# Kernel tuning notes

Hardware: AMD Instinct MI355X
Metric: run time of the kernel (lower is better)

## Reference

```python
import jax, jax.numpy as jnp
import numpy as np

B, NORB, N_UP, N_DN, HIDDEN = 1024, 128, 32, 32, 4096


def setup_inputs() -> dict:
    rng = np.random.default_rng(0)
    # Build valid occupancy configs: exactly N_UP up-electrons (bit 0) and
    # N_DN down-electrons (bit 1) per sample. Encoding: 0=empty,1=up,2=dn,3=updn.
    up_order = np.argsort(rng.random((B, NORB)), axis=1)
    dn_order = np.argsort(rng.random((B, NORB)), axis=1)
    up_bit = np.zeros((B, NORB), np.int32)
    dn_bit = np.zeros((B, NORB), np.int32)
    np.put_along_axis(up_bit, up_order[:, :N_UP], 1, axis=1)
    np.put_along_axis(dn_bit, dn_order[:, :N_DN], 1, axis=1)
    x = jnp.asarray(up_bit + 2 * dn_bit, dtype=jnp.int32)

    key = jax.random.key(0)
    k1, k2, k3 = jax.random.split(key, 3)
    orbitals = jax.random.normal(k1, (NORB, N_UP), jnp.float32)
    W1 = jax.random.normal(k2, (4 * NORB, HIDDEN), jnp.float32) / np.sqrt(4 * NORB)
    b1 = jnp.zeros((HIDDEN,), jnp.float32)
    W2 = jax.random.normal(k3, (HIDDEN, NORB * N_UP), jnp.float32) / np.sqrt(HIDDEN)
    b2 = jnp.zeros((NORB * N_UP,), jnp.float32)
    return {"x": x, "orbitals": orbitals, "W1": W1, "b1": b1, "W2": W2, "b2": b2}


def _occupancies_to_electrons(x, n_up, n_dn):
    # Per-spin sorted positions of occupied orbitals. Stable argsort on the
    # inverted mask keeps occupied sites first, in ascending orbital order.
    up_mask = (x & 1) == 1
    dn_mask = (x & 2) == 2
    y_up = jnp.argsort(jnp.where(up_mask, 0, 1), axis=-1, stable=True)[:, :n_up]
    y_dn = jnp.argsort(jnp.where(dn_mask, 0, 1), axis=-1, stable=True)[:, :n_dn]
    return y_up, y_dn


def reference(x, orbitals, W1, b1, W2, b2):
    Bsz, norb = x.shape
    n_up = orbitals.shape[1]

    # correction_fun: MLP on one-hot config -> [B, norb, n_up]
    h = jax.nn.one_hot(x, 4, dtype=W1.dtype).reshape(Bsz, -1)  # [B, 4*norb]
    h = jax.nn.relu(h @ W1 + b1)                               # [B, hidden]
    corrections = (h @ W2 + b2).reshape(Bsz, norb, n_up)       # [B, norb, n_up]

    y_up, y_dn = _occupancies_to_electrons(x, n_up, n_up)
    y_up = y_up[..., None]  # [B, n_up, 1]
    y_dn = y_dn[..., None]

    # gather orbital rows + correction rows per electron (spin-symmetric orbitals)
    phi_up = jnp.take_along_axis(orbitals[None], y_up, axis=1)  # [B, n_up, n_up]
    phi_dn = jnp.take_along_axis(orbitals[None], y_dn, axis=1)
    d_up = jnp.take_along_axis(corrections, y_up, axis=1)
    d_dn = jnp.take_along_axis(corrections, y_dn, axis=1)

    s_up, log_det_up = jnp.linalg.slogdet(phi_up + d_up)
    s_dn, log_det_dn = jnp.linalg.slogdet(phi_dn + d_dn)
    return log_det_up + log_det_dn + jnp.log(s_up * s_dn + 0j)  # complex [B]
```

## Files before the change

kernel.cpp:

```cpp
#include <hip/hip_runtime.h>
#include <cmath>

#define B_SZ  1024
#define NORB  128
#define NUP   32
#define HID   4096
#define NCORR (NORB * NUP)
#define K1    (4 * NORB)

typedef short    bf16x8 __attribute__((ext_vector_type(8)));
typedef _Float16 f16x8  __attribute__((ext_vector_type(8)));
typedef float    f32x4  __attribute__((ext_vector_type(4)));

__device__ __forceinline__ unsigned short f2bf_rne(float f) {
    unsigned int u = __float_as_uint(f);
    u += 0x7FFFu + ((u >> 16) & 1u);
    return (unsigned short)(u >> 16);
}

__global__ __launch_bounds__(256) void k_splitW(const float* __restrict__ W,
                                                unsigned short* __restrict__ Bph,
                                                unsigned short* __restrict__ Bpl,
                                                int ktTot) {
    __shared__ float tile[64][33];
    int n0 = blockIdx.x * 32, k0 = blockIdx.y * 64;
    int t = threadIdx.x;

    int rl = t >> 3, c4 = (t & 7) * 4;
#pragma unroll
    for (int i = 0; i < 2; ++i) {
        int kl = rl + 32 * i;
        float4 v = *(const float4*)(W + (size_t)(k0 + kl) * 4096 + n0 + c4);
        tile[kl][c4 + 0] = v.x; tile[kl][c4 + 1] = v.y;
        tile[kl][c4 + 2] = v.z; tile[kl][c4 + 3] = v.w;
    }
    __syncthreads();

    int nl = t & 31, kg = t >> 5;
    int nt = (n0 + nl) >> 4;
    int kt = (k0 >> 5) + (kg >> 2);
    int lane_o = (kg & 3) * 16 + (nl & 15);
    size_t o = (((size_t)nt * ktTot + kt) * 64 + lane_o) * 8;

    unsigned short hi8[8], lo8[8];
#pragma unroll
    for (int j = 0; j < 8; ++j) {
        float v = tile[kg * 8 + j][nl];
        unsigned short hi = f2bf_rne(v);
        float fhi = __uint_as_float((unsigned int)hi << 16);
        hi8[j] = hi;
        lo8[j] = f2bf_rne(v - fhi);
    }
    *(bf16x8*)(Bph + o) = *(bf16x8*)hi8;
    *(bf16x8*)(Bpl + o) = *(bf16x8*)lo8;
}

__global__ __launch_bounds__(256, 2) void k_hidden3(const int* __restrict__ x,
                                                    const unsigned short* __restrict__ Bph,
                                                    const unsigned short* __restrict__ Bpl,
                                                    const float* __restrict__ b1,
                                                    _Float16* __restrict__ h16) {
    __shared__ unsigned int sxp[64][8];
    __shared__ unsigned short BF[2][4][4][512];
    __shared__ float Ht[64][132];

    int n0 = blockIdx.x * 128;
    int m0 = blockIdx.y * 64;
    int t = threadIdx.x;
    int w = t >> 6, lane = t & 63;
    int lm = lane & 15, kq = lane >> 4;
    int wn = w * 32;

#pragma unroll
    for (int i = 0; i < 2; ++i) {
        int id = t + 256 * i;
        int row = id >> 3, d = id & 7;
        const int* src = x + (size_t)(m0 + row) * NORB + d * 16;
        unsigned int dw = 0;
#pragma unroll
        for (int b = 0; b < 16; ++b) dw |= ((unsigned int)(src[b] & 3)) << (2 * b);
        sxp[row][d] = dw;
    }

    int nt0 = (n0 + wn) >> 4;
    const unsigned short* bh0 = Bph + (size_t)nt0 * (16 * 512) + (size_t)lane * 8;
    const unsigned short* bh1 = Bph + (size_t)(nt0 + 1) * (16 * 512) + (size_t)lane * 8;
    const unsigned short* bl0 = Bpl + (size_t)nt0 * (16 * 512) + (size_t)lane * 8;
    const unsigned short* bl1 = Bpl + (size_t)(nt0 + 1) * (16 * 512) + (size_t)lane * 8;

    f32x4 acc[4][2] = {};

    bf16x8 r0 = *(const bf16x8*)(bh0);
    bf16x8 r1 = *(const bf16x8*)(bh1);
    bf16x8 r2 = *(const bf16x8*)(bl0);
    bf16x8 r3 = *(const bf16x8*)(bl1);
    bf16x8 r4 = *(const bf16x8*)(bh0 + 512);
    bf16x8 r5 = *(const bf16x8*)(bh1 + 512);
    bf16x8 r6 = *(const bf16x8*)(bl0 + 512);
    bf16x8 r7 = *(const bf16x8*)(bl1 + 512);

    __syncthreads();

    for (int p = 0; p < 8; ++p) {
        if (p) __syncthreads();

        *(bf16x8*)&BF[0][w][0][lane * 8] = r0;
        *(bf16x8*)&BF[0][w][1][lane * 8] = r1;
        *(bf16x8*)&BF[0][w][2][lane * 8] = r2;
        *(bf16x8*)&BF[0][w][3][lane * 8] = r3;
        *(bf16x8*)&BF[1][w][0][lane * 8] = r4;
        *(bf16x8*)&BF[1][w][1][lane * 8] = r5;
        *(bf16x8*)&BF[1][w][2][lane * 8] = r6;
        *(bf16x8*)&BF[1][w][3][lane * 8] = r7;
        __syncthreads();

        int kn = (p + 1 < 8) ? p + 1 : 7;
        r0 = *(const bf16x8*)(bh0 + (2 * kn) * 512);
        r1 = *(const bf16x8*)(bh1 + (2 * kn) * 512);
        r2 = *(const bf16x8*)(bl0 + (2 * kn) * 512);
        r3 = *(const bf16x8*)(bl1 + (2 * kn) * 512);
        r4 = *(const bf16x8*)(bh0 + (2 * kn + 1) * 512);
        r5 = *(const bf16x8*)(bh1 + (2 * kn + 1) * 512);
        r6 = *(const bf16x8*)(bl0 + (2 * kn + 1) * 512);
        r7 = *(const bf16x8*)(bl1 + (2 * kn + 1) * 512);
        __builtin_amdgcn_sched_barrier(0);

#pragma unroll
        for (int s = 0; s < 2; ++s) {
            int kt = 2 * p + s;
            int i0 = kt * 8 + kq * 2;
            int dwIdx = i0 >> 4;
            int sh = (i0 & 15) * 2;
            bf16x8 af[4];
#pragma unroll
            for (int fm = 0; fm < 4; ++fm) {
                unsigned int dw = sxp[fm * 16 + lm][dwIdx];
                unsigned int c01 = (dw >> sh) & 0xFu;
                union { bf16x8 v; unsigned long long u[2]; } a;
                a.u[0] = 0x3F80ULL << ((c01 & 3u) * 16);
                a.u[1] = 0x3F80ULL << ((c01 >> 2) * 16);
                af[fm] = a.v;
            }

            bf16x8 b0h = *(const bf16x8*)&BF[s][w][0][lane * 8];
            bf16x8 b1h = *(const bf16x8*)&BF[s][w][1][lane * 8];
            bf16x8 b0l = *(const bf16x8*)&BF[s][w][2][lane * 8];
            bf16x8 b1l = *(const bf16x8*)&BF[s][w][3][lane * 8];

#pragma unroll
            for (int fm = 0; fm < 4; ++fm) {
                acc[fm][0] = __builtin_amdgcn_mfma_f32_16x16x32_bf16(af[fm], b0h, acc[fm][0], 0, 0, 0);
                acc[fm][0] = __builtin_amdgcn_mfma_f32_16x16x32_bf16(af[fm], b0l, acc[fm][0], 0, 0, 0);
                acc[fm][1] = __builtin_amdgcn_mfma_f32_16x16x32_bf16(af[fm], b1h, acc[fm][1], 0, 0, 0);
                acc[fm][1] = __builtin_amdgcn_mfma_f32_16x16x32_bf16(af[fm], b1l, acc[fm][1], 0, 0, 0);
            }
        }
    }

    __syncthreads();
#pragma unroll
    for (int fm = 0; fm < 4; ++fm)
#pragma unroll
        for (int fn = 0; fn < 2; ++fn) {
            int n = wn + fn * 16 + lm;
            float bv = b1[n0 + n];
#pragma unroll
            for (int r = 0; r < 4; ++r)
                Ht[fm * 16 + kq * 4 + r][n] = fmaxf(acc[fm][fn][r] + bv, 0.f);
        }
    __syncthreads();

    size_t mt0 = (size_t)(m0 >> 4), kt0 = (size_t)(n0 >> 5);
#pragma unroll
    for (int fi = 0; fi < 4; ++fi) {
        int f = w * 4 + fi;
        int mt = f >> 2, ktn = f & 3;
        int m = mt * 16 + lm;
        int kn = ktn * 32 + kq * 8;
        float4 v0 = *(const float4*)&Ht[m][kn];
        float4 v1 = *(const float4*)&Ht[m][kn + 4];
        float vv[8] = {v0.x, v0.y, v0.z, v0.w, v1.x, v1.y, v1.z, v1.w};
        f16x8 o16;
#pragma unroll
        for (int j = 0; j < 8; ++j) o16[j] = (_Float16)vv[j];
        size_t o = (((mt0 + mt) * 128 + (kt0 + ktn)) * 64 + lane) * 8;
        *(f16x8*)(h16 + o) = o16;
    }
}

__global__ __launch_bounds__(256) void k_hidden_f32(const int* __restrict__ x,
                                                    const float* __restrict__ W1,
                                                    const float* __restrict__ b1,
                                                    float* __restrict__ h) {
    int b = blockIdx.x, tid = threadIdx.x;
    __shared__ int sx[NORB];
    if (tid < NORB) sx[tid] = x[b * NORB + tid];
    __syncthreads();
    float acc[16];
#pragma unroll
    for (int u = 0; u < 16; ++u) acc[u] = b1[tid + 256 * u];
    for (int i = 0; i < NORB; ++i) {
        const float* row = W1 + (size_t)(4 * i + sx[i]) * HID;
#pragma unroll
        for (int u = 0; u < 16; ++u) acc[u] += row[tid + 256 * u];
    }
    float* hb = h + (size_t)b * HID;
#pragma unroll
    for (int u = 0; u < 16; ++u) hb[tid + 256 * u] = fmaxf(acc[u], 0.f);
}

__global__ __launch_bounds__(256, 2) void k_gemm10(const _Float16* __restrict__ Ap,
                                                   const float* __restrict__ W2f,
                                                   const float* __restrict__ bias,
                                                   float* __restrict__ C) {
    __shared__ _Float16 AF[2][2][4][512];

    int n0 = blockIdx.x * 128;
    int m0 = blockIdx.y * 64;
    int t = threadIdx.x;
    int w = t >> 6, lane = t & 63;
    int lm = lane & 15, kq = lane >> 4;
    int wn = w * 32;

    int mt0 = m0 >> 4;
    int nt0 = (n0 + wn) >> 4;

    const _Float16* ag = Ap + (size_t)(mt0 + w) * 65536 + (size_t)lane * 8;
    const float* bW = W2f + (size_t)(kq * 8) * 4096 + (size_t)nt0 * 16 + lm;

    f32x4 accH[4][2] = {}, accL[4][2] = {};

    f16x8 r0 = *(const f16x8*)(ag);
    f16x8 r1 = *(const f16x8*)(ag + 512);
    float cB[4][8];
#pragma unroll
    for (int s = 0; s < 2; ++s)
#pragma unroll
        for (int c = 0; c < 2; ++c)
#pragma unroll
            for (int j = 0; j < 8; ++j)
                cB[s * 2 + c][j] = bW[(size_t)(s * 32 + j) * 4096 + c * 16];

    for (int ktp = 0; ktp < 64; ++ktp) {
        int buf = ktp & 1;
        *(f16x8*)&AF[buf][0][w][lane * 8] = r0;
        *(f16x8*)&AF[buf][1][w][lane * 8] = r1;
        __syncthreads();

        int kn = (ktp + 1 < 64) ? ktp + 1 : 63;
        f16x8 nr0 = *(const f16x8*)(ag + (size_t)(2 * kn) * 512);
        f16x8 nr1 = *(const f16x8*)(ag + (size_t)(2 * kn + 1) * 512);
        float nB[4][8];
#pragma unroll
        for (int s = 0; s < 2; ++s)
#pragma unroll
            for (int c = 0; c < 2; ++c)
#pragma unroll
                for (int j = 0; j < 8; ++j)
                    nB[s * 2 + c][j] =
                        bW[(size_t)((2 * kn + s) * 32 + j) * 4096 + c * 16];
        __builtin_amdgcn_sched_barrier(0);

        f16x8 a0[4], a1[4];
#pragma unroll
        for (int fm = 0; fm < 4; ++fm) {
            a0[fm] = *(const f16x8*)&AF[buf][0][fm][lane * 8];
            a1[fm] = *(const f16x8*)&AF[buf][1][fm][lane * 8];
        }

#pragma unroll
        for (int s = 0; s < 2; ++s) {
            f16x8 bh0, bl0, bh1, bl1;
#pragma unroll
            for (int j = 0; j < 8; ++j) {
                float v0 = cB[s * 2 + 0][j];
                _Float16 h0 = (_Float16)v0;
                bh0[j] = h0;
                bl0[j] = (_Float16)((v0 - (float)h0) * 2048.0f);
                float v1 = cB[s * 2 + 1][j];
                _Float16 h1 = (_Float16)v1;
                bh1[j] = h1;
                bl1[j] = (_Float16)((v1 - (float)h1) * 2048.0f);
            }
#pragma unroll
            for (int fm = 0; fm < 4; ++fm) {
                f16x8 a = s ? a1[fm] : a0[fm];
                accH[fm][0] = __builtin_amdgcn_mfma_f32_16x16x32_f16(a, bh0, accH[fm][0], 0, 0, 0);
                accL[fm][0] = __builtin_amdgcn_mfma_f32_16x16x32_f16(a, bl0, accL[fm][0], 0, 0, 0);
                accH[fm][1] = __builtin_amdgcn_mfma_f32_16x16x32_f16(a, bh1, accH[fm][1], 0, 0, 0);
                accL[fm][1] = __builtin_amdgcn_mfma_f32_16x16x32_f16(a, bl1, accL[fm][1], 0, 0, 0);
            }
        }

        r0 = nr0; r1 = nr1;
#pragma unroll
        for (int f = 0; f < 4; ++f)
#pragma unroll
            for (int j = 0; j < 8; ++j) cB[f][j] = nB[f][j];
    }

    const float ls = 1.0f / 2048.0f;
#pragma unroll
    for (int fm = 0; fm < 4; ++fm)
#pragma unroll
        for (int fn = 0; fn < 2; ++fn) {
            int n = n0 + wn + fn * 16 + lm;
            float bv = bias[n];
#pragma unroll
            for (int r = 0; r < 4; ++r) {
                int m = m0 + fm * 16 + kq * 4 + r;
                C[(size_t)m * NCORR + n] = accH[fm][fn][r] + ls * accL[fm][fn][r] + bv;
            }
        }
}

#define BM 64
#define BN 64
#define BK 32
__global__ __launch_bounds__(256) void k_gemm(const float* __restrict__ A,
                                              const float* __restrict__ Bm,
                                              const float* __restrict__ bias,
                                              float* __restrict__ C) {
    __shared__ float As[BK][68];
    __shared__ float Bs[BK][BN];
    int n0 = blockIdx.x * BN, m0 = blockIdx.y * BM;
    int tid = threadIdx.x;
    int tm = tid >> 4, tn = tid & 15;
    int am = tid >> 3, ak = (tid & 7) * 4;
    int bk = tid >> 4, bn = (tid & 15) * 4;
    float acc[4][4] = {};
    for (int k0 = 0; k0 < HID; k0 += BK) {
#pragma unroll
        for (int s = 0; s < 2; ++s) {
            int m = am + 32 * s;
            float4 v = *(const float4*)(A + (size_t)(m0 + m) * HID + k0 + ak);
            As[ak + 0][m] = v.x; As[ak + 1][m] = v.y;
            As[ak + 2][m] = v.z; As[ak + 3][m] = v.w;
        }
#pragma unroll
        for (int s = 0; s < 2; ++s) {
            int k = bk + 16 * s;
            float4 v = *(const float4*)(Bm + (size_t)(k0 + k) * NCORR + n0 + bn);
            *(float4*)&Bs[k][bn] = v;
        }
        __syncthreads();
#pragma unroll
        for (int kk = 0; kk < BK; ++kk) {
            float4 a = *(const float4*)&As[kk][tm * 4];
            float4 bv = *(const float4*)&Bs[kk][tn * 4];
            float av[4] = {a.x, a.y, a.z, a.w};
            float bb[4] = {bv.x, bv.y, bv.z, bv.w};
#pragma unroll
            for (int i = 0; i < 4; ++i)
#pragma unroll
                for (int j = 0; j < 4; ++j) acc[i][j] += av[i] * bb[j];
        }
        __syncthreads();
    }
#pragma unroll
    for (int i = 0; i < 4; ++i) {
        int m = m0 + tm * 4 + i;
        float4 o;
        o.x = acc[i][0] + bias[n0 + tn * 4 + 0];
        o.y = acc[i][1] + bias[n0 + tn * 4 + 1];
        o.z = acc[i][2] + bias[n0 + tn * 4 + 2];
        o.w = acc[i][3] + bias[n0 + tn * 4 + 3];
        *(float4*)(C + (size_t)m * NCORR + n0 + tn * 4) = o;
    }
}

__global__ __launch_bounds__(128) void k_det(const int* __restrict__ x,
                                             const float* __restrict__ orbitals,
                                             const float* __restrict__ corr,
                                             float* __restrict__ out,
                                             int imag_off) {
    int b = blockIdx.x, tid = threadIdx.x;
    __shared__ int sx[NORB];
    __shared__ int yup[NUP], ydn[NUP];
    __shared__ float M[2][NUP][NUP + 1];
    __shared__ float rlog[2];
    __shared__ int rneg[2];

    sx[tid] = x[b * NORB + tid];
    __syncthreads();

    int occ = sx[tid];
    if (occ & 1) {
        int r = 0;
        for (int i = 0; i < tid; ++i) r += sx[i] & 1;
        yup[r] = tid;
    }
    if (occ & 2) {
        int r = 0;
        for (int i = 0; i < tid; ++i) r += (sx[i] >> 1) & 1;
        ydn[r] = tid;
    }
    __syncthreads();

    const float* cb = corr + (size_t)b * NCORR;
    for (int idx = tid; idx < 2 * NUP * NUP; idx += 128) {
        int s = idx >> 10;
        int i = (idx >> 5) & 31;
        int j = idx & 31;
        int r = s ? ydn[i] : yup[i];
        M[s][i][j] = orbitals[r * NUP + j] + cb[r * NUP + j];
    }
    __syncthreads();

    int wv = tid >> 6, lane = tid & 63;
    float (*Mm)[NUP + 1] = M[wv];
    float logdet = 0.f;
    int neg = 0;

    for (int k = 0; k < NUP; ++k) {
        float v = (lane >= k && lane < NUP) ? fabsf(Mm[lane][k]) : -1.f;
        int pi = lane;
#pragma unroll
        for (int off = 32; off > 0; off >>= 1) {
            float v2 = __shfl_down(v, off);
            int p2 = __shfl_down(pi, off);
            if (v2 > v) { v = v2; pi = p2; }
        }
        int p = __shfl(pi, 0);

        if (p != k) {
            if (lane < NUP) {
                float t1 = Mm[k][lane];
                Mm[k][lane] = Mm[p][lane];
                Mm[p][lane] = t1;
            }
            neg ^= 1;
        }
        __syncthreads();

        float pv = Mm[k][k];
        logdet += logf(fabsf(pv));
        if (pv < 0.f) neg ^= 1;

        int row = k + 1 + (lane & 31);
        int half = lane >> 5;
        if (row < NUP) {
            float f = Mm[row][k] / pv;
            for (int j = k + 1 + half; j < NUP; j += 2)
                Mm[row][j] -= f * Mm[k][j];
        }
        __syncthreads();
    }

    if (lane == 0) { rlog[wv] = logdet; rneg[wv] = neg; }
    __syncthreads();
    if (tid == 0) {
        out[b] = rlog[0] + rlog[1];
        if (imag_off > 0)
            out[imag_off + b] =
                (rneg[0] ^ rneg[1]) ? 3.14159265358979323846f : 0.f;
    }
}

extern "C" void kernel_launch(void* const* d_in, const int* in_sizes, int n_in,
                              void* d_out, int out_size, void* d_ws, size_t ws_size,
                              hipStream_t stream) {
    const int*   x        = (const int*)d_in[0];
    const float* orbitals = (const float*)d_in[1];
    const float* W1       = (const float*)d_in[2];
    const float* b1       = (const float*)d_in[3];
    const float* W2       = (const float*)d_in[4];
    const float* b2       = (const float*)d_in[5];
    float* out = (float*)d_out;
    int imag_off = (out_size == 2 * B_SZ) ? B_SZ : 0;

    const size_t need = (size_t)32 * 1024 * 1024;
    if (ws_size >= need) {
        _Float16* h16  = (_Float16*)d_ws;
        float*    corr = (float*)(h16 + (size_t)B_SZ * HID);

        unsigned short* W1ph = (unsigned short*)corr;
        unsigned short* W1pl = W1ph + (size_t)K1 * HID;

        k_splitW<<<dim3(HID / 32, K1 / 64), 256, 0, stream>>>(W1, W1ph, W1pl, 16);

        k_hidden3<<<dim3(HID / 128, B_SZ / 64), 256, 0, stream>>>(x, W1ph, W1pl, b1, h16);

        dim3 g2(NCORR / 128, B_SZ / 64);
        k_gemm10<<<g2, 256, 0, stream>>>(h16, W2, b2, corr);

        k_det<<<B_SZ, 128, 0, stream>>>(x, orbitals, corr, out, imag_off);
    } else {
        float* h    = (float*)d_ws;
        float* corr = h + (size_t)B_SZ * HID;
        k_hidden_f32<<<B_SZ, 256, 0, stream>>>(x, W1, b1, h);
        dim3 g2(NCORR / BN, B_SZ / BM);
        k_gemm<<<g2, 256, 0, stream>>>(h, W2, b2, corr);
        k_det<<<B_SZ, 128, 0, stream>>>(x, orbitals, corr, out, imag_off);
    }
}
```

Measured before the change: 245.1 us.

## Stage W2 tiles through swizzled LDS with coalesced float4 loads in GEMM

```diff
diff --git a/kernel.cpp b/kernel.cpp
--- a/kernel.cpp
+++ b/kernel.cpp
@@ -209,10 +209,11 @@
     for (int u = 0; u < 16; ++u) hb[tid + 256 * u] = fmaxf(acc[u], 0.f);
 }
 
-__global__ __launch_bounds__(256, 2) void k_gemm10(const _Float16* __restrict__ Ap,
+__global__ __launch_bounds__(256, 2) void k_gemm12(const _Float16* __restrict__ Ap,
                                                    const float* __restrict__ W2f,
                                                    const float* __restrict__ bias,
                                                    float* __restrict__ C) {
+    __shared__ float    Wt[2][64][128];
     __shared__ _Float16 AF[2][2][4][512];
 
     int n0 = blockIdx.x * 128;
@@ -223,26 +224,32 @@
     int wn = w * 32;
 
     int mt0 = m0 >> 4;
-    int nt0 = (n0 + wn) >> 4;
 
     const _Float16* ag = Ap + (size_t)(mt0 + w) * 65536 + (size_t)lane * 8;
-    const float* bW = W2f + (size_t)(kq * 8) * 4096 + (size_t)nt0 * 16 + lm;
+
+    int srow = t >> 2;
+    int scg  = t & 3;
+    int skq  = (srow >> 3) & 3;
+    const float* wg0 = W2f + (size_t)srow * 4096 + n0;
+
+    int g0  = 8 * w + (lm >> 2) + 4 * kq;
+    int co0 = ((g0 & 31) << 2) | (lm & 3);
+    int co1 = (((g0 + 4) & 31) << 2) | (lm & 3);
 
     f32x4 accH[4][2] = {}, accL[4][2] = {};
 
     f16x8 r0 = *(const f16x8*)(ag);
     f16x8 r1 = *(const f16x8*)(ag + 512);
-    float cB[4][8];
-#pragma unroll
-    for (int s = 0; s < 2; ++s)
-#pragma unroll
-        for (int c = 0; c < 2; ++c)
-#pragma unroll
-            for (int j = 0; j < 8; ++j)
-                cB[s * 2 + c][j] = bW[(size_t)(s * 32 + j) * 4096 + c * 16];
+    float4 wr[8];
+#pragma unroll
+    for (int q = 0; q < 8; ++q)
+        wr[q] = *(const float4*)(wg0 + ((scg + 4 * q) << 2));
 
     for (int ktp = 0; ktp < 64; ++ktp) {
         int buf = ktp & 1;
+#pragma unroll
+        for (int q = 0; q < 8; ++q)
+            *(float4*)&Wt[buf][srow][((scg + 4 * q + 4 * skq) & 31) << 2] = wr[q];
         *(f16x8*)&AF[buf][0][w][lane * 8] = r0;
         *(f16x8*)&AF[buf][1][w][lane * 8] = r1;
         __syncthreads();
@@ -250,15 +257,11 @@
         int kn = (ktp + 1 < 64) ? ktp + 1 : 63;
         f16x8 nr0 = *(const f16x8*)(ag + (size_t)(2 * kn) * 512);
         f16x8 nr1 = *(const f16x8*)(ag + (size_t)(2 * kn + 1) * 512);
-        float nB[4][8];
-#pragma unroll
-        for (int s = 0; s < 2; ++s)
-#pragma unroll
-            for (int c = 0; c < 2; ++c)
-#pragma unroll
-                for (int j = 0; j < 8; ++j)
-                    nB[s * 2 + c][j] =
-                        bW[(size_t)((2 * kn + s) * 32 + j) * 4096 + c * 16];
+        const float* wgn = wg0 + (size_t)kn * 262144;
+        float4 nw[8];
+#pragma unroll
+        for (int q = 0; q < 8; ++q)
+            nw[q] = *(const float4*)(wgn + ((scg + 4 * q) << 2));
         __builtin_amdgcn_sched_barrier(0);
 
         f16x8 a0[4], a1[4];
@@ -270,14 +273,15 @@
 
 #pragma unroll
         for (int s = 0; s < 2; ++s) {
+            const float* wrow = &Wt[buf][s * 32 + kq * 8][0];
             f16x8 bh0, bl0, bh1, bl1;
 #pragma unroll
             for (int j = 0; j < 8; ++j) {
-                float v0 = cB[s * 2 + 0][j];
+                float v0 = wrow[j * 128 + co0];
                 _Float16 h0 = (_Float16)v0;
                 bh0[j] = h0;
                 bl0[j] = (_Float16)((v0 - (float)h0) * 2048.0f);
-                float v1 = cB[s * 2 + 1][j];
+                float v1 = wrow[j * 128 + co1];
                 _Float16 h1 = (_Float16)v1;
                 bh1[j] = h1;
                 bl1[j] = (_Float16)((v1 - (float)h1) * 2048.0f);
@@ -294,9 +298,7 @@
 
         r0 = nr0; r1 = nr1;
 #pragma unroll
-        for (int f = 0; f < 4; ++f)
-#pragma unroll
-            for (int j = 0; j < 8; ++j) cB[f][j] = nB[f][j];
+        for (int q = 0; q < 8; ++q) wr[q] = nw[q];
     }
 
     const float ls = 1.0f / 2048.0f;
@@ -482,7 +484,7 @@
         k_hidden3<<<dim3(HID / 128, B_SZ / 64), 256, 0, stream>>>(x, W1ph, W1pl, b1, h16);
 
         dim3 g2(NCORR / 128, B_SZ / 64);
-        k_gemm10<<<g2, 256, 0, stream>>>(h16, W2, b2, corr);
+        k_gemm12<<<g2, 256, 0, stream>>>(h16, W2, b2, corr);
 
         k_det<<<B_SZ, 128, 0, stream>>>(x, orbitals, corr, out, imag_off);
     } else {
```

Measured after the change: 484.0 us. +97.5%, slower.
